# Kernel tuning notes

Hardware: AMD Instinct MI355X
Metric: run time of the kernel (lower is better)

## Reference

```python
import jax, jax.numpy as jnp
import numpy as np

B, S, V, H, O = 64, 1024, 32000, 1024, 128


def setup_inputs() -> dict:
    key = jax.random.key(0)
    ks = jax.random.split(key, 10)
    s = 1.0 / np.sqrt(H)
    return {
        "x": jax.random.randint(ks[0], (B, S), 0, V, dtype=jnp.int32),
        "emb": jax.random.normal(ks[1], (V, H), jnp.float32),
        "W_ih": jax.random.normal(ks[2], (4 * H, H), jnp.float32) * s,
        "W_hh": jax.random.normal(ks[3], (4 * H, H), jnp.float32) * s,
        "b_ih": jax.random.normal(ks[4], (4 * H,), jnp.float32) * s,
        "b_hh": jax.random.normal(ks[5], (4 * H,), jnp.float32) * s,
        "fc_W": jax.random.normal(ks[6], (O, H), jnp.float32) * s,
        "fc_b": jax.random.normal(ks[7], (O,), jnp.float32) * s,
        "h0": jax.random.normal(ks[8], (B, H), jnp.float32),
        "c0": jax.random.normal(ks[9], (B, H), jnp.float32),
    }


def lstm_forward(x, emb, W_ih, W_hh, b_ih, b_hh, fc_W, fc_b, h0, c0):
    # Embedding gather: [B,S,H]
    xe = emb[x]
    # Precompute input contribution to gates for ALL timesteps at once: [S,B,4H]
    gates_x = jnp.einsum("bsh,gh->sbg", xe, W_ih) + b_ih + b_hh

    def step(carry, gx):
        h, c = carry
        gates = gx + h @ W_hh.T  # [B,4H]
        i, f, g, o = jnp.split(gates, 4, axis=-1)  # PyTorch ifgo order
        i = jax.nn.sigmoid(i)
        f = jax.nn.sigmoid(f)
        g = jnp.tanh(g)
        o = jax.nn.sigmoid(o)
        c = f * c + i * g
        h = o * jnp.tanh(c)
        return (h, c), None

    (h_last, _), _ = jax.lax.scan(step, (h0, c0), gates_x)
    # fc on last timestep output only
    return h_last @ fc_W.T + fc_b  # [B,O]


def reference(x, emb, W_ih, W_hh, b_ih, b_hh, fc_W, fc_b, h0, c0):
    return lstm_forward(x, emb, W_ih, W_hh, b_ih, b_hh, fc_W, fc_b, h0, c0)
```

## Files before the change

kernel.cpp:

```cpp
#include <hip/hip_runtime.h>
#include <stdint.h>

#define BB 64
#define SS 1024
#define VV 32000
#define HH 1024
#define NWG 256
#define NTHR 512
#define BBHH ((size_t)BB * HH)

typedef unsigned short u16;
typedef unsigned int u32;
typedef unsigned long long u64;
typedef short bf8 __attribute__((ext_vector_type(8)));
typedef float f32x4 __attribute__((ext_vector_type(4)));

#define WL_BYTES  131072
#define RED_BYTES (16 * 16 * 17 * 4)
#define LDS_TOTAL (WL_BYTES + RED_BYTES)

#define CTR_STRIDE 32
#define CTR_BYTES  (NWG * CTR_STRIDE * 4)

static __device__ __forceinline__ u16 f2bf(float f) {
    union { float f; uint32_t u; } v; v.f = f;
    return (u16)((v.u + 0x7fffu + ((v.u >> 16) & 1u)) >> 16);
}
static __device__ __forceinline__ float bf2f(u16 u) {
    union { uint32_t u; float f; } v; v.u = ((uint32_t)u) << 16; return v.f;
}
static __device__ __forceinline__ float fsig(float x) {
    return __builtin_amdgcn_rcpf(1.f + __expf(-x));
}
static __device__ __forceinline__ float ftanh(float x) {
    return 1.f - 2.f * __builtin_amdgcn_rcpf(1.f + __expf(2.f * x));
}
static __device__ __forceinline__ bf8 pack2(f32x4 a, f32x4 b) {
    union { u32 w[4]; bf8 v; } r;
    asm("v_cvt_pk_bf16_f32 %0, %1, %2" : "=v"(r.w[0]) : "v"(a[0]), "v"(a[1]));
    asm("v_cvt_pk_bf16_f32 %0, %1, %2" : "=v"(r.w[1]) : "v"(a[2]), "v"(a[3]));
    asm("v_cvt_pk_bf16_f32 %0, %1, %2" : "=v"(r.w[2]) : "v"(b[0]), "v"(b[1]));
    asm("v_cvt_pk_bf16_f32 %0, %1, %2" : "=v"(r.w[3]) : "v"(b[2]), "v"(b[3]));
    return r.v;
}

__global__ __launch_bounds__(256) void emb_cvt(
    const float* __restrict__ emb, u16* __restrict__ dst)
{
    size_t i = ((size_t)blockIdx.x * 256 + threadIdx.x) * 8;
    f32x4 a = *(const f32x4*)(emb + i);
    f32x4 b = *(const f32x4*)(emb + i + 4);
    *(bf8*)(dst + i) = pack2(a, b);
}

__global__ __launch_bounds__(256) void init_misc(
    const float* __restrict__ h0, u16* __restrict__ hseq0, u32* __restrict__ ctr)
{
    int i = blockIdx.x * 256 + threadIdx.x;
    if (i < BB * HH) hseq0[i] = f2bf(h0[i]);
    if (i < NWG * CTR_STRIDE) ctr[i] = 0u;
}

__global__ __launch_bounds__(NTHR, 1) void lstm_persist(
    const int*   __restrict__ x,
    const float* __restrict__ emb,
    const u16*   __restrict__ embbf,
    const float* __restrict__ Wih,
    const float* __restrict__ Whh,
    const float* __restrict__ bih,
    const float* __restrict__ bhh,
    const float* __restrict__ c0,
    u16*         __restrict__ hseq,
    u32*         __restrict__ ctr,
    int cached,
    int embf)
{
    extern __shared__ char smem[];
    u16* WL = (u16*)smem;
    float (*red)[16][17] = (float (*)[16][17])(smem + WL_BYTES);

    const int tid  = threadIdx.x;
    const int wv   = tid >> 6;
    const int lane = tid & 63;
    const int n16  = lane & 15;
    const int quad = lane >> 4;
    const int bh   = (blockIdx.x & 7) >> 2;
    const int cb   = ((blockIdx.x >> 3) << 2) | (blockIdx.x & 3);

    for (int u = tid; u < 8192; u += NTHR) {
        int ln  = u & 63;
        int kb  = (u >> 6) & 31;
        int nh  = (u >> 11) & 1;
        int mat = u >> 12;
        int rl  = nh * 16 + (ln & 15);
        int q   = rl >> 3, j = rl & 7;
        const float* src = (mat ? Whh : Wih)
                         + (size_t)(q * HH + cb * 8 + j) * HH + kb * 32 + (ln >> 4) * 8;
        u16* dst = WL + (size_t)u * 8;
        #pragma unroll
        for (int e = 0; e < 8; ++e) dst[e] = f2bf(src[e]);
    }

    float bias[4] = {0.f, 0.f, 0.f, 0.f};
    float creg = 0.f;
    int eb = 0, ech = 0;
    if (tid < 256) {
        int mhe = tid >> 7, m = (tid >> 3) & 15, j = tid & 7;
        eb  = bh * 32 + mhe * 16 + m;
        ech = cb * 8 + j;
        #pragma unroll
        for (int q = 0; q < 4; ++q) bias[q] = bih[q * HH + ech] + bhh[q * HH + ech];
    }

    const int mh = wv >> 2, kh = wv & 3;
    const int ab = bh * 32 + mh * 16 + n16;
    const u16* WLx0 = WL + ((size_t)(0 * 32 + kh * 8) * 512) + lane * 8;
    const u16* WLx1 = WL + ((size_t)(1 * 32 + kh * 8) * 512) + lane * 8;
    const u16* WLr0 = WL + ((size_t)(2 * 32 + kh * 8) * 512) + lane * 8;
    const u16* WLr1 = WL + ((size_t)(3 * 32 + kh * 8) * 512) + lane * 8;

    __syncthreads();

    u32* myctr = ctr + (size_t)(bh * 128 + cb) * CTR_STRIDE;
    u32* poll0 = ctr + (size_t)(bh * 128 + lane) * CTR_STRIDE;
    u32* poll1 = ctr + (size_t)(bh * 128 + 64 + lane) * CTR_STRIDE;

    f32x4 accx0, accx1;
    auto xphase = [&](int xr) {
        f32x4 a0 = {0.f, 0.f, 0.f, 0.f}, a1 = {0.f, 0.f, 0.f, 0.f};
        if (embf) {
            const u16* ep = embbf + (size_t)xr * HH + kh * 256 + quad * 8;
            #pragma unroll
            for (int t = 0; t < 8; ++t) {
                bf8 av = *(const bf8*)(ep + t * 32);
                bf8 b0 = *(const bf8*)(WLx0 + t * 512);
                bf8 b1 = *(const bf8*)(WLx1 + t * 512);
                a0 = __builtin_amdgcn_mfma_f32_16x16x32_bf16(av, b0, a0, 0, 0, 0);
                a1 = __builtin_amdgcn_mfma_f32_16x16x32_bf16(av, b1, a1, 0, 0, 0);
            }
        } else {
            const float* ep = emb + (size_t)xr * HH + kh * 256 + quad * 8;
            #pragma unroll
            for (int t = 0; t < 8; ++t) {
                bf8 av = pack2(*(const f32x4*)(ep + t * 32),
                               *(const f32x4*)(ep + t * 32 + 4));
                bf8 b0 = *(const bf8*)(WLx0 + t * 512);
                bf8 b1 = *(const bf8*)(WLx1 + t * 512);
                a0 = __builtin_amdgcn_mfma_f32_16x16x32_bf16(av, b0, a0, 0, 0, 0);
                a1 = __builtin_amdgcn_mfma_f32_16x16x32_bf16(av, b1, a1, 0, 0, 0);
            }
        }
        accx0 = a0; accx1 = a1;
    };
    xphase(x[(size_t)ab * SS + 0]);

    for (int s = 0; s < SS; ++s) {
        const bool more = (s + 1 < SS);
        const int  ri   = cached ? s : (s & 1);
        const int  wi   = cached ? (s + 1) : ((s + 1) & 1);

        int xr_next = 0;
        if (more) xr_next = x[(size_t)ab * SS + (s + 1)];

        {
            const u16* hp = hseq + (size_t)ri * BBHH
                          + (size_t)ab * HH + kh * 256 + quad * 8;
            bf8 hv[8];
            if (cached) {
                #pragma unroll
                for (int t = 0; t < 8; ++t) hv[t] = *(const bf8*)(hp + t * 32);
            } else {
                #pragma unroll
                for (int t = 0; t < 8; ++t) {
                    union { u64 q[2]; bf8 v; } av;
                    av.q[0] = __hip_atomic_load((const u64*)(hp + t * 32),
                                  __ATOMIC_RELAXED, __HIP_MEMORY_SCOPE_AGENT);
                    av.q[1] = __hip_atomic_load((const u64*)(hp + t * 32 + 4),
                                  __ATOMIC_RELAXED, __HIP_MEMORY_SCOPE_AGENT);
                    hv[t] = av.v;
                }
            }
            f32x4 a0 = accx0, a1 = accx1;
            #pragma unroll
            for (int t = 0; t < 8; ++t) {
                bf8 b0 = *(const bf8*)(WLr0 + t * 512);
                bf8 b1 = *(const bf8*)(WLr1 + t * 512);
                a0 = __builtin_amdgcn_mfma_f32_16x16x32_bf16(hv[t], b0, a0, 0, 0, 0);
                a1 = __builtin_amdgcn_mfma_f32_16x16x32_bf16(hv[t], b1, a1, 0, 0, 0);
            }
            const int w2 = wv * 2;
            #pragma unroll
            for (int r = 0; r < 4; ++r) {
                red[w2 + 0][quad * 4 + r][n16] = a0[r];
                red[w2 + 1][quad * 4 + r][n16] = a1[r];
            }
        }
        __syncthreads();

        if (tid < 256) {
            const int mhe = tid >> 7, m = (tid >> 3) & 15, j = tid & 7;
            float g[4];
            #pragma unroll
            for (int q = 0; q < 4; ++q) {
                const int nh = q >> 1, nn = (q & 1) * 8 + j;
                float acc = bias[q];
                #pragma unroll
                for (int k = 0; k < 4; ++k)
                    acc += red[(mhe * 4 + k) * 2 + nh][m][nn];
                g[q] = acc;
            }
            float ig = fsig(g[0]);
            float fg = fsig(g[1]);
            float gv = ftanh(g[2]);
            float og = fsig(g[3]);
            float cp = (s == 0) ? c0[(size_t)eb * HH + ech] : creg;
            float cn = fg * cp + ig * gv;
            creg = cn;
            u32 hv = f2bf(og * ftanh(cn));
            u32 p1 = (u32)__shfl_xor((int)hv, 1);
            u32 w  = hv | (p1 << 16);
            u32 wp = (u32)__shfl_xor((int)w, 2);
            if ((tid & 3) == 0) {
                u64 dv = (u64)w | ((u64)wp << 32);
                u16* hd = hseq + (size_t)wi * BBHH + (size_t)eb * HH + ech;
                __hip_atomic_store((u64*)hd, dv,
                                   __ATOMIC_RELAXED, __HIP_MEMORY_SCOPE_AGENT);
            }
        }

        if (more) {
            if (wv < 4) {
                __builtin_amdgcn_s_waitcnt(0);
                if (lane == 0)
                    __hip_atomic_fetch_add(myctr, 1u, __ATOMIC_RELAXED,
                                           __HIP_MEMORY_SCOPE_AGENT);
            }
            xphase(xr_next);
            if (wv == 7) {
                const u32 tgt = 4u * (u32)(s + 1);
                for (;;) {
                    u32 a = __hip_atomic_load(poll0, __ATOMIC_RELAXED,
                                              __HIP_MEMORY_SCOPE_AGENT);
                    u32 b = __hip_atomic_load(poll1, __ATOMIC_RELAXED,
                                              __HIP_MEMORY_SCOPE_AGENT);
                    if (__all((a >= tgt) && (b >= tgt))) break;
                    __builtin_amdgcn_s_sleep(1);
                }
            }
            __syncthreads();
        }
    }
}

__global__ __launch_bounds__(128) void fc_kernel(
    const u16*   __restrict__ h,
    const float* __restrict__ fcW,
    const float* __restrict__ fcb,
    float*       __restrict__ out)
{
    int b = blockIdx.x;
    int o = threadIdx.x;
    const u16*   hp = h + (size_t)b * HH;
    const float* wp = fcW + (size_t)o * HH;
    float acc = 0.f;
    for (int k = 0; k < HH; k += 8) {
        bf8 hv = *(const bf8*)(hp + k);
        #pragma unroll
        for (int e = 0; e < 8; ++e)
            acc += bf2f((u16)hv[e]) * wp[k + e];
    }
    out[(size_t)b * 128 + o] = acc + fcb[o];
}

extern "C" void kernel_launch(void* const* d_in, const int* in_sizes, int n_in,
                              void* d_out, int out_size, void* d_ws, size_t ws_size,
                              hipStream_t stream) {
    const int*   x   = (const int*)d_in[0];
    const float* emb = (const float*)d_in[1];
    const float* Wih = (const float*)d_in[2];
    const float* Whh = (const float*)d_in[3];
    const float* bih = (const float*)d_in[4];
    const float* bhh = (const float*)d_in[5];
    const float* fcW = (const float*)d_in[6];
    const float* fcb = (const float*)d_in[7];
    const float* h0  = (const float*)d_in[8];
    const float* c0  = (const float*)d_in[9];

    const size_t hbytes    = BBHH * sizeof(u16);
    const size_t base_need = (size_t)(SS + 1) * hbytes + CTR_BYTES;
    const size_t emb_bytes = (size_t)VV * HH * sizeof(u16);
    const size_t full_need = base_need + emb_bytes;

    const int cached = (ws_size >= base_need) ? 1 : 0;
    const int embf   = (ws_size >= full_need) ? 1 : 0;
    const int nbuf   = cached ? (SS + 1) : 2;

    u16* hseq  = (u16*)d_ws;
    u32* ctr   = (u32*)((char*)d_ws + (size_t)nbuf * hbytes);
    u16* embbf = (u16*)((char*)d_ws + (size_t)(SS + 1) * hbytes + CTR_BYTES);

    hipFuncSetAttribute((const void*)lstm_persist,
                        hipFuncAttributeMaxDynamicSharedMemorySize, LDS_TOTAL);

    if (embf)
        emb_cvt<<<VV * HH / (256 * 8), 256, 0, stream>>>(emb, embbf);
    init_misc<<<256, 256, 0, stream>>>(h0, hseq, ctr);
    lstm_persist<<<NWG, NTHR, LDS_TOTAL, stream>>>(x, emb, embbf, Wih, Whh,
                                                   bih, bhh, c0, hseq, ctr,
                                                   cached, embf);
    fc_kernel<<<BB, 128, 0, stream>>>(hseq + (size_t)(cached ? SS : 0) * BBHH,
                                      fcW, fcb, (float*)d_out);
}
```

Baseline: 5.044 ms.

## Move input-projection MFMAs after barrier and prefetch next embedding row in registers

For the cached/bf16-embedding path, a specialized loop now issues the h loads first, then computes the x-projection MFMAs for the current step inside the critical path while the h loads are in flight, and prefetches the next token's embedding row into registers. Previously the x-phase ran between the counter increment and the poll barrier, overlapping with the cross-workgroup wait. This trades that wait-overlap for hiding h-load latency behind x MFMAs and removing embedding-load latency from the step. Risk: extra MFMA work now sits on the serial recurrence path and register pressure rises.

```diff
diff --git a/kernel.cpp b/kernel.cpp
--- a/kernel.cpp
+++ b/kernel.cpp
@@ -126,128 +126,203 @@
     u32* poll1 = ctr + (size_t)(bh * 128 + 64 + lane) * CTR_STRIDE;
 
     f32x4 accx0, accx1;
-    auto xphase = [&](int xr) {
-        f32x4 a0 = {0.f, 0.f, 0.f, 0.f}, a1 = {0.f, 0.f, 0.f, 0.f};
-        if (embf) {
-            const u16* ep = embbf + (size_t)xr * HH + kh * 256 + quad * 8;
+
+    auto epilogue = [&](int s, int wi) {
+        const int mhe = tid >> 7, m = (tid >> 3) & 15, j = tid & 7;
+        float g[4];
+        #pragma unroll
+        for (int q = 0; q < 4; ++q) {
+            const int nh = q >> 1, nn = (q & 1) * 8 + j;
+            float acc = bias[q];
             #pragma unroll
-            for (int t = 0; t < 8; ++t) {
-                bf8 av = *(const bf8*)(ep + t * 32);
-                bf8 b0 = *(const bf8*)(WLx0 + t * 512);
-                bf8 b1 = *(const bf8*)(WLx1 + t * 512);
-                a0 = __builtin_amdgcn_mfma_f32_16x16x32_bf16(av, b0, a0, 0, 0, 0);
-                a1 = __builtin_amdgcn_mfma_f32_16x16x32_bf16(av, b1, a1, 0, 0, 0);
-            }
-        } else {
-            const float* ep = emb + (size_t)xr * HH + kh * 256 + quad * 8;
+            for (int k = 0; k < 4; ++k)
+                acc += red[(mhe * 4 + k) * 2 + nh][m][nn];
+            g[q] = acc;
+        }
+        float ig = fsig(g[0]);
+        float fg = fsig(g[1]);
+        float gv = ftanh(g[2]);
+        float og = fsig(g[3]);
+        float cp = (s == 0) ? c0[(size_t)eb * HH + ech] : creg;
+        float cn = fg * cp + ig * gv;
+        creg = cn;
+        u32 hv = f2bf(og * ftanh(cn));
+        u32 p1 = (u32)__shfl_xor((int)hv, 1);
+        u32 w  = hv | (p1 << 16);
+        u32 wp = (u32)__shfl_xor((int)w, 2);
+        if ((tid & 3) == 0) {
+            u64 dv = (u64)w | ((u64)wp << 32);
+            u16* hd = hseq + (size_t)wi * BBHH + (size_t)eb * HH + ech;
+            __hip_atomic_store((u64*)hd, dv,
+                               __ATOMIC_RELAXED, __HIP_MEMORY_SCOPE_AGENT);
+        }
+    };
+    auto wave7_poll = [&](u32 tgt) {
+        for (;;) {
+            u32 a = __hip_atomic_load(poll0, __ATOMIC_RELAXED,
+                                      __HIP_MEMORY_SCOPE_AGENT);
+            u32 b = __hip_atomic_load(poll1, __ATOMIC_RELAXED,
+                                      __HIP_MEMORY_SCOPE_AGENT);
+            if (__all((a >= tgt) && (b >= tgt))) break;
+            __builtin_amdgcn_s_sleep(1);
+        }
+    };
+
+    if (cached && embf) {
+        int tok_cur = x[(size_t)ab * SS + 0];
+        int tok_nxt = x[(size_t)ab * SS + 1];
+        bf8 E[8];
+        {
+            const u16* ep = embbf + (size_t)tok_cur * HH + kh * 256 + quad * 8;
             #pragma unroll
-            for (int t = 0; t < 8; ++t) {
-                bf8 av = pack2(*(const f32x4*)(ep + t * 32),
-                               *(const f32x4*)(ep + t * 32 + 4));
-                bf8 b0 = *(const bf8*)(WLx0 + t * 512);
-                bf8 b1 = *(const bf8*)(WLx1 + t * 512);
-                a0 = __builtin_amdgcn_mfma_f32_16x16x32_bf16(av, b0, a0, 0, 0, 0);
-                a1 = __builtin_amdgcn_mfma_f32_16x16x32_bf16(av, b1, a1, 0, 0, 0);
-            }
-        }
-        accx0 = a0; accx1 = a1;
-    };
-    xphase(x[(size_t)ab * SS + 0]);
-
-    for (int s = 0; s < SS; ++s) {
-        const bool more = (s + 1 < SS);
-        const int  ri   = cached ? s : (s & 1);
-        const int  wi   = cached ? (s + 1) : ((s + 1) & 1);
-
-        int xr_next = 0;
-        if (more) xr_next = x[(size_t)ab * SS + (s + 1)];
-
-        {
-            const u16* hp = hseq + (size_t)ri * BBHH
+            for (int t = 0; t < 8; ++t) E[t] = *(const bf8*)(ep + t * 32);
+        }
+        for (int s = 0; s < SS; ++s) {
+            const bool more = (s + 1 < SS);
+
+            const u16* hp = hseq + (size_t)s * BBHH
                           + (size_t)ab * HH + kh * 256 + quad * 8;
             bf8 hv[8];
-            if (cached) {
-                #pragma unroll
-                for (int t = 0; t < 8; ++t) hv[t] = *(const bf8*)(hp + t * 32);
+            #pragma unroll
+            for (int t = 0; t < 8; ++t) hv[t] = *(const bf8*)(hp + t * 32);
+            __builtin_amdgcn_sched_barrier(0);
+
+            {
+                f32x4 a0 = {0.f, 0.f, 0.f, 0.f}, a1 = {0.f, 0.f, 0.f, 0.f};
+                #pragma unroll
+                for (int t = 0; t < 8; ++t) {
+                    bf8 b0 = *(const bf8*)(WLx0 + t * 512);
+                    bf8 b1 = *(const bf8*)(WLx1 + t * 512);
+                    a0 = __builtin_amdgcn_mfma_f32_16x16x32_bf16(E[t], b0, a0, 0, 0, 0);
+                    a1 = __builtin_amdgcn_mfma_f32_16x16x32_bf16(E[t], b1, a1, 0, 0, 0);
+                }
+                accx0 = a0; accx1 = a1;
+            }
+
+            if (more) {
+                const u16* ep = embbf + (size_t)tok_nxt * HH + kh * 256 + quad * 8;
+                #pragma unroll
+                for (int t = 0; t < 8; ++t) E[t] = *(const bf8*)(ep + t * 32);
+            }
+            tok_cur = tok_nxt;
+            if (s + 2 < SS) tok_nxt = x[(size_t)ab * SS + (s + 2)];
+
+            {
+                f32x4 a0 = accx0, a1 = accx1;
+                #pragma unroll
+                for (int t = 0; t < 8; ++t) {
+                    bf8 b0 = *(const bf8*)(WLr0 + t * 512);
+                    bf8 b1 = *(const bf8*)(WLr1 + t * 512);
+                    a0 = __builtin_amdgcn_mfma_f32_16x16x32_bf16(hv[t], b0, a0, 0, 0, 0);
+                    a1 = __builtin_amdgcn_mfma_f32_16x16x32_bf16(hv[t], b1, a1, 0, 0, 0);
+                }
+                const int w2 = wv * 2;
+                #pragma unroll
+                for (int r = 0; r < 4; ++r) {
+                    red[w2 + 0][quad * 4 + r][n16] = a0[r];
+                    red[w2 + 1][quad * 4 + r][n16] = a1[r];
+                }
+            }
+            __syncthreads();
+
+            if (tid < 256) epilogue(s, s + 1);
+
+            if (more) {
+                if (wv < 4) {
+                    __builtin_amdgcn_s_waitcnt(0);
+                    if (lane == 0)
+                        __hip_atomic_fetch_add(myctr, 1u, __ATOMIC_RELAXED,
+                                               __HIP_MEMORY_SCOPE_AGENT);
+                }
+                if (wv == 7) wave7_poll(4u * (u32)(s + 1));
+                __syncthreads();
+            }
+        }
+    } else {
+        auto xphase = [&](int xr) {
+            f32x4 a0 = {0.f, 0.f, 0.f, 0.f}, a1 = {0.f, 0.f, 0.f, 0.f};
+            if (embf) {
+                const u16* ep = embbf + (size_t)xr * HH + kh * 256 + quad * 8;
+                #pragma unroll
+                for (int t = 0; t < 8; ++t) {
+                    bf8 av = *(const bf8*)(ep + t * 32);
+                    bf8 b0 = *(const bf8*)(WLx0 + t * 512);
+                    bf8 b1 = *(const bf8*)(WLx1 + t * 512);
+                    a0 = __builtin_amdgcn_mfma_f32_16x16x32_bf16(av, b0, a0, 0, 0, 0);
+                    a1 = __builtin_amdgcn_mfma_f32_16x16x32_bf16(av, b1, a1, 0, 0, 0);
+                }
             } else {
-                #pragma unroll
-                for (int t = 0; t < 8; ++t) {
-                    union { u64 q[2]; bf8 v; } av;
-                    av.q[0] = __hip_atomic_load((const u64*)(hp + t * 32),
-                                  __ATOMIC_RELAXED, __HIP_MEMORY_SCOPE_AGENT);
-                    av.q[1] = __hip_atomic_load((const u64*)(hp + t * 32 + 4),
-                                  __ATOMIC_RELAXED, __HIP_MEMORY_SCOPE_AGENT);
-                    hv[t] = av.v;
-                }
-            }
-            f32x4 a0 = accx0, a1 = accx1;
-            #pragma unroll
-            for (int t = 0; t < 8; ++t) {
-                bf8 b0 = *(const bf8*)(WLr0 + t * 512);
-                bf8 b1 = *(const bf8*)(WLr1 + t * 512);
-                a0 = __builtin_amdgcn_mfma_f32_16x16x32_bf16(hv[t], b0, a0, 0, 0, 0);
-                a1 = __builtin_amdgcn_mfma_f32_16x16x32_bf16(hv[t], b1, a1, 0, 0, 0);
-            }
-            const int w2 = wv * 2;
-            #pragma unroll
-            for (int r = 0; r < 4; ++r) {
-                red[w2 + 0][quad * 4 + r][n16] = a0[r];
-                red[w2 + 1][quad * 4 + r][n16] = a1[r];
-            }
-        }
-        __syncthreads();
-
-        if (tid < 256) {
-            const int mhe = tid >> 7, m = (tid >> 3) & 15, j = tid & 7;
-            float g[4];
-            #pragma unroll
-            for (int q = 0; q < 4; ++q) {
-                const int nh = q >> 1, nn = (q & 1) * 8 + j;
-                float acc = bias[q];
-                #pragma unroll
-                for (int k = 0; k < 4; ++k)
-                    acc += red[(mhe * 4 + k) * 2 + nh][m][nn];
-                g[q] = acc;
-            }
-            float ig = fsig(g[0]);
-            float fg = fsig(g[1]);
-            float gv = ftanh(g[2]);
-            float og = fsig(g[3]);
-            float cp = (s == 0) ? c0[(size_t)eb * HH + ech] : creg;
-            float cn = fg * cp + ig * gv;
-            creg = cn;
-            u32 hv = f2bf(og * ftanh(cn));
-            u32 p1 = (u32)__shfl_xor((int)hv, 1);
-            u32 w  = hv | (p1 << 16);
-            u32 wp = (u32)__shfl_xor((int)w, 2);
-            if ((tid & 3) == 0) {
-                u64 dv = (u64)w | ((u64)wp << 32);
-                u16* hd = hseq + (size_t)wi * BBHH + (size_t)eb * HH + ech;
-                __hip_atomic_store((u64*)hd, dv,
-                                   __ATOMIC_RELAXED, __HIP_MEMORY_SCOPE_AGENT);
-            }
-        }
-
-        if (more) {
-            if (wv < 4) {
-                __builtin_amdgcn_s_waitcnt(0);
-                if (lane == 0)
-                    __hip_atomic_fetch_add(myctr, 1u, __ATOMIC_RELAXED,
-                                           __HIP_MEMORY_SCOPE_AGENT);
-            }
-            xphase(xr_next);
-            if (wv == 7) {
-                const u32 tgt = 4u * (u32)(s + 1);
-                for (;;) {
-                    u32 a = __hip_atomic_load(poll0, __ATOMIC_RELAXED,
-                                              __HIP_MEMORY_SCOPE_AGENT);
-                    u32 b = __hip_atomic_load(poll1, __ATOMIC_RELAXED,
-                                              __HIP_MEMORY_SCOPE_AGENT);
-                    if (__all((a >= tgt) && (b >= tgt))) break;
-                    __builtin_amdgcn_s_sleep(1);
+                const float* ep = emb + (size_t)xr * HH + kh * 256 + quad * 8;
+                #pragma unroll
+                for (int t = 0; t < 8; ++t) {
+                    bf8 av = pack2(*(const f32x4*)(ep + t * 32),
+                                   *(const f32x4*)(ep + t * 32 + 4));
+                    bf8 b0 = *(const bf8*)(WLx0 + t * 512);
+                    bf8 b1 = *(const bf8*)(WLx1 + t * 512);
+                    a0 = __builtin_amdgcn_mfma_f32_16x16x32_bf16(av, b0, a0, 0, 0, 0);
+                    a1 = __builtin_amdgcn_mfma_f32_16x16x32_bf16(av, b1, a1, 0, 0, 0);
+                }
+            }
+            accx0 = a0; accx1 = a1;
+        };
+        xphase(x[(size_t)ab * SS + 0]);
+
+        for (int s = 0; s < SS; ++s) {
+            const bool more = (s + 1 < SS);
+            const int  ri   = cached ? s : (s & 1);
+            const int  wi   = cached ? (s + 1) : ((s + 1) & 1);
+
+            int xr_next = 0;
+            if (more) xr_next = x[(size_t)ab * SS + (s + 1)];
+
+            {
+                const u16* hp = hseq + (size_t)ri * BBHH
+                              + (size_t)ab * HH + kh * 256 + quad * 8;
+                bf8 hv[8];
+                if (cached) {
+                    #pragma unroll
+                    for (int t = 0; t < 8; ++t) hv[t] = *(const bf8*)(hp + t * 32);
+                } else {
+                    #pragma unroll
+                    for (int t = 0; t < 8; ++t) {
+                        union { u64 q[2]; bf8 v; } av;
+                        av.q[0] = __hip_atomic_load((const u64*)(hp + t * 32),
+                                      __ATOMIC_RELAXED, __HIP_MEMORY_SCOPE_AGENT);
+                        av.q[1] = __hip_atomic_load((const u64*)(hp + t * 32 + 4),
+                                      __ATOMIC_RELAXED, __HIP_MEMORY_SCOPE_AGENT);
+                        hv[t] = av.v;
+                    }
+                }
+                f32x4 a0 = accx0, a1 = accx1;
+                #pragma unroll
+                for (int t = 0; t < 8; ++t) {
+                    bf8 b0 = *(const bf8*)(WLr0 + t * 512);
+                    bf8 b1 = *(const bf8*)(WLr1 + t * 512);
+                    a0 = __builtin_amdgcn_mfma_f32_16x16x32_bf16(hv[t], b0, a0, 0, 0, 0);
+                    a1 = __builtin_amdgcn_mfma_f32_16x16x32_bf16(hv[t], b1, a1, 0, 0, 0);
+                }
+                const int w2 = wv * 2;
+                #pragma unroll
+                for (int r = 0; r < 4; ++r) {
+                    red[w2 + 0][quad * 4 + r][n16] = a0[r];
+                    red[w2 + 1][quad * 4 + r][n16] = a1[r];
                 }
             }
             __syncthreads();
+
+            if (tid < 256) epilogue(s, wi);
+
+            if (more) {
+                if (wv < 4) {
+                    __builtin_amdgcn_s_waitcnt(0);
+                    if (lane == 0)
+                        __hip_atomic_fetch_add(myctr, 1u, __ATOMIC_RELAXED,
+                                               __HIP_MEMORY_SCOPE_AGENT);
+                }
+                xphase(xr_next);
+                if (wv == 7) wave7_poll(4u * (u32)(s + 1));
+                __syncthreads();
+            }
         }
     }
 }
```

Result: slower. 7.538 ms (+49.4%).
